# Kernel optimization log

Hardware: AMD Instinct MI355X
Metric: run time of the kernel (lower is better)

## Reference

```python
import jax, jax.numpy as jnp
import numpy as np

N, D, V, T = 2048, 64, 32000, 512
K_WTA = 256
X_DECAY, U_DECAY = 0.97, 0.97
SPIKE_RATE = 0.01
FORGET_ETA = 0.01
HOMEO_TAU = 1.0
GAMMA_MAX = 1.0


def ln_row(z, eps=1e-6):
    # torch .std is unbiased (ddof=1)
    m = z.mean(-1, keepdims=True)
    s = z.std(-1, ddof=1, keepdims=True)
    return (z - m) / (s + eps)


def setup_inputs() -> dict:
    key = jax.random.key(0)
    ks = jax.random.split(key, 6)
    return {
        "tokens": jax.random.randint(ks[0], (T,), 0, V),
        "spike_u": jax.random.uniform(ks[1], (T, N), dtype=jnp.float32),
        "E": jax.random.normal(ks[2], (D, N), dtype=jnp.float32) / np.sqrt(N).astype(np.float32),
        "Dx": jax.random.normal(ks[3], (N, D), dtype=jnp.float32) / np.sqrt(D).astype(np.float32),
        "Dy": jax.random.normal(ks[4], (N, D), dtype=jnp.float32) / np.sqrt(D).astype(np.float32),
        "token_emb": jax.random.normal(ks[5], (V, D), dtype=jnp.float32) / np.sqrt(D).astype(np.float32),
    }


def reference(tokens, spike_u, E, Dx, Dy, token_emb):
    def step(carry, inp):
        x, rho = carry
        tok, u = inp
        v_prev = token_emb[tok]                                   # (D,)
        x_t = X_DECAY * x + jax.nn.relu(Dx @ v_prev)              # (N,)
        x_t = x_t / (jnp.sum(jnp.abs(x_t)) + 1e-6)                # L1 normalize
        a_hat = ln_row(rho @ x_t)                                 # (D,) ln_before_Dy
        # branches=4 with elementwise softplus == softplus on full matvec
        y_core = jax.nn.softplus(Dy @ a_hat)                      # (N,)
        y_core = y_core + (u < SPIKE_RATE).astype(y_core.dtype)   # spike noise
        # k-WTA: keep top K_WTA entries
        _, idx = jax.lax.top_k(y_core, K_WTA)
        mask = jnp.zeros((N,), bool).at[idx].set(True)
        y_core = y_core * mask.astype(y_core.dtype)
        y_t = jax.nn.relu(y_core) * jax.nn.relu(x_t)
        # homeostasis (torch uses .item() -> constant scale)
        s = y_t.sum()
        scale = jnp.where(s > 1e-8, jnp.minimum(1.0, HOMEO_TAU / (s + 1e-8)), 1.0)
        y_t = y_t * jax.lax.stop_gradient(scale)
        v_star = ln_row(E @ y_t)                                  # (D,)
        # surprisal gain (torch uses .item() -> constant)
        p = jax.nn.softmax(v_star)
        H = -(p * jnp.log(p + 1e-12)).sum()
        gain = jnp.minimum(GAMMA_MAX, H / jnp.log(jnp.float32(D) + 1e-6) * GAMMA_MAX)
        gain = jax.lax.stop_gradient(gain)
        # dynamic top-k on x_t via rank masking (jit-safe data-dependent k)
        k_dyn = jnp.clip((N * (0.05 + 0.25 * gain)).astype(jnp.int32), 1, N)
        order = jnp.argsort(-x_t)
        ranks = jnp.zeros((N,), jnp.int32).at[order].set(jnp.arange(N, dtype=jnp.int32))
        x_t = x_t * (ranks < k_dyn).astype(x_t.dtype)
        # local forgetting on inactive columns, then Hebbian update
        inactive = (x_t <= 0).astype(rho.dtype)
        rho = rho * (1.0 - FORGET_ETA * inactive[None, :])
        rho = U_DECAY * (rho + gain * jnp.outer(v_prev, x_t))
        return (x_t, rho), v_star

    init = (jnp.zeros((N,), jnp.float32), jnp.zeros((D, N), jnp.float32))
    (_, _), v_stack = jax.lax.scan(step, init, (tokens, spike_u))
    return v_stack  # (T, D)
```

## Files before the change

### kernel.cpp

```cpp
#include <hip/hip_runtime.h>
#include <math.h>

#define NB   16
#define NTH  256
#define CH   128
#define NN   2048
#define DD   64
#define TT   512
#define KWTA 256
#define PA   65
#define PB   132

struct __align__(128) BarFlag { unsigned v; unsigned pad[31]; };
__device__ BarFlag g_flag[NB];
__device__ __align__(16) float  g_rf[NB][DD];
__device__ __align__(16) float  g_ef[NB][DD];
__device__ __align__(16) double g_L1[NB];
__device__ __align__(16) double g_s [NB];
__device__ __align__(16) float  g_xg[NN];
__device__ __align__(16) float  g_yg[NN];

__global__ void bdh_init() { if (threadIdx.x < NB) g_flag[threadIdx.x].v = 0u; }

__device__ __forceinline__ void grid_barrier(unsigned& epoch) {
  epoch += 1u;
  __syncthreads();
  if (threadIdx.x < 64) {
    if (threadIdx.x == 0) {
      __threadfence();
      __hip_atomic_store(&g_flag[blockIdx.x].v, epoch, __ATOMIC_RELAXED,
                         __HIP_MEMORY_SCOPE_AGENT);
    }
    const int i = (int)threadIdx.x;
    for (;;) {
      const bool ok = (i >= NB) ||
        (__hip_atomic_load(&g_flag[i].v, __ATOMIC_RELAXED,
                           __HIP_MEMORY_SCOPE_AGENT) >= epoch);
      if (__all(ok)) break;
      __builtin_amdgcn_s_sleep(1);
    }
    __builtin_amdgcn_fence(__ATOMIC_ACQUIRE, "agent");
  }
  __syncthreads();
}

__device__ __forceinline__ double wredd(double v) {
  #pragma unroll
  for (int off = 32; off > 0; off >>= 1) v += __shfl_xor(v, off, 64);
  return v;
}
__device__ __forceinline__ float wredf(float v) {
  #pragma unroll
  for (int off = 32; off > 0; off >>= 1) v += __shfl_xor(v, off, 64);
  return v;
}

__device__ void select_topk(const unsigned* __restrict__ keys, int K, int n0, int tid,
                            float* __restrict__ keep,
                            unsigned* __restrict__ hist,
                            unsigned* __restrict__ wsum,
                            int* __restrict__ misc)
{
  const int wave = tid >> 6, lane = tid & 63;
  const int sub = tid & 7;
  uint4* h4 = (uint4*)hist;
  unsigned prefix = 0u, pmask = 0u;
  int remK = K;
  for (int lev = 0; lev < 4; ++lev) {
    const int shf = 24 - 8*lev;
    const uint4 z = {0u,0u,0u,0u};
    h4[tid] = z; h4[tid + 256] = z;
    __syncthreads();
    #pragma unroll
    for (int j = 0; j < 8; ++j)
      if ((keys[j] & pmask) == prefix)
        atomicAdd(&hist[(((keys[j] >> shf) & 255u) << 3) + sub], 1u);
    __syncthreads();
    const uint4 a = h4[tid*2], bq = h4[tid*2 + 1];
    const unsigned c = a.x+a.y+a.z+a.w + bq.x+bq.y+bq.z+bq.w;
    unsigned s = c;
    #pragma unroll
    for (int off = 1; off < 64; off <<= 1) {
      unsigned o = __shfl_down(s, off, 64);
      if (lane + off < 64) s += o;
    }
    if (lane == 0) wsum[wave] = s;
    __syncthreads();
    unsigned hi = 0;
    for (int w = wave + 1; w < 4; ++w) hi += wsum[w];
    const unsigned A = s + hi;
    if (A >= (unsigned)remK && (A - c) < (unsigned)remK) {
      misc[0] = tid;
      misc[1] = remK - (int)(A - c);
    }
    __syncthreads();
    prefix |= ((unsigned)misc[0]) << shf;
    pmask  |= (255u << shf);
    remK = misc[1];
  }
  const unsigned thr = prefix;
  const unsigned R = (unsigned)remK;
  int lc[8]; int cnt = 0;
  #pragma unroll
  for (int j = 0; j < 8; ++j) { lc[j] = cnt; cnt += (keys[j] == thr) ? 1 : 0; }
  unsigned e = (unsigned)cnt;
  #pragma unroll
  for (int off = 1; off < 64; off <<= 1) {
    unsigned o = __shfl_up(e, off, 64);
    if (lane >= off) e += o;
  }
  if (lane == 63) wsum[4 + wave] = e;
  __syncthreads();
  unsigned base = 0;
  for (int w = 0; w < wave; ++w) base += wsum[4 + w];
  const unsigned excl = base + e - (unsigned)cnt;
  #pragma unroll
  for (int j = 0; j < 8; ++j) {
    const int g = tid*8 + j;
    const unsigned gg = (unsigned)(g - n0);
    if (gg < (unsigned)CH) {
      const bool kp = (keys[j] > thr) || ((keys[j] == thr) && (excl + (unsigned)lc[j] < R));
      keep[gg] = kp ? 1.0f : 0.0f;
    }
  }
  __syncthreads();
}

__global__ void __launch_bounds__(NTH)
bdh_main(const int* __restrict__ tokens, const float* __restrict__ spike_u,
         const float* __restrict__ Emat, const float* __restrict__ Dx,
         const float* __restrict__ Dy, const float* __restrict__ temb,
         float* __restrict__ out)
{
  __shared__ float sh_rho[DD][PB];
  __shared__ float sh_Dx[CH][PA];
  __shared__ float sh_Dy[CH][PA];
  __shared__ float sh_E [DD][PB];
  __shared__ int   sh_tok[TT];
  __shared__ float sh_v[2][DD];
  __shared__ float sh_xstate[CH];
  __shared__ float sh_xtun[CH];
  __shared__ float sh_xt[CH];
  __shared__ float sh_y[CH];
  __shared__ float sh_yt[CH];
  __shared__ float sh_ahat[DD];
  __shared__ float sh_keep[CH];
  __shared__ float sh_ffac[CH];
  __shared__ unsigned sh_hist[256*8];
  __shared__ unsigned sh_wsum[8];
  __shared__ int sh_misc[4];
  __shared__ float sh_fmisc[4];
  __shared__ double sh_dred[8];
  __shared__ double sh_rd[4][DD];

  const int tid  = threadIdx.x;
  const int b    = blockIdx.x;
  const int n0   = b * CH;
  const int i2   = tid >> 1;
  const int p2   = tid & 1;
  const int d4   = tid >> 2;
  const int p4   = tid & 3;
  const int lane = tid & 63;
  const int wv   = tid >> 6;
  unsigned epoch = 0u;

  for (int k = tid; k < TT; k += NTH) sh_tok[k] = tokens[k];
  for (int k = tid; k < DD*PB; k += NTH) (&sh_rho[0][0])[k] = 0.0f;
  if (tid < CH) sh_xstate[tid] = 0.0f;
  for (int r = wv; r < CH; r += 4) {
    sh_Dx[r][lane] = Dx[(size_t)(n0 + r)*DD + lane];
    sh_Dy[r][lane] = Dy[(size_t)(n0 + r)*DD + lane];
  }
  for (int r = wv; r < DD; r += 4) {
    sh_E[r][lane]      = Emat[(size_t)r*NN + n0 + lane];
    sh_E[r][lane + 64] = Emat[(size_t)r*NN + n0 + lane + 64];
  }
  __syncthreads();
  if (tid < DD) sh_v[0][tid] = temb[(size_t)sh_tok[0]*DD + tid];
  __syncthreads();

  for (int t = 0; t < TT; ++t) {
    const int par = t & 1;

    float spu = 0.0f;
    if (p2 == 0) spu = spike_u[(size_t)t*NN + n0 + i2];
    if (t + 1 < TT && tid < DD)
      sh_v[par ^ 1][tid] = temb[(size_t)sh_tok[t + 1]*DD + tid];

    float d1 = 0.0f;
    {
      const float* dxr = &sh_Dx[i2][p2*32];
      const float* vv  = &sh_v[par][p2*32];
      #pragma unroll
      for (int j = 0; j < 32; ++j) d1 += dxr[j] * vv[j];
    }
    d1 += __shfl_xor(d1, 1, 64);
    float xnew = 0.0f;
    if (p2 == 0) {
      xnew = 0.97f * sh_xstate[i2] + fmaxf(d1, 0.0f);
      sh_xtun[i2] = xnew;
    }
    {
      double v = (p2 == 0) ? (double)fabsf(xnew) : 0.0;
      v = wredd(v);
      if (lane == 0) sh_dred[wv] = v;
      __syncthreads();
      if (tid == 0) g_L1[b] = sh_dred[0] + sh_dred[1] + sh_dred[2] + sh_dred[3];
    }
    float qa = 0.0f;
    {
      const float* rr = &sh_rho[d4][0];
      #pragma unroll
      for (int j = 0; j < 32; ++j) { const int c = p4 + 4*j; qa += rr[c] * sh_xtun[c]; }
    }
    qa += __shfl_xor(qa, 1, 64);
    qa += __shfl_xor(qa, 2, 64);
    if (p4 == 0) g_rf[b][d4] = qa;
    grid_barrier(epoch);

    {
      double acc = 0.0;
      #pragma unroll
      for (int j = 0; j < 4; ++j) acc += (double)g_rf[(wv<<2) + j][lane];
      sh_rd[wv][lane] = acc;
    }
    if (tid < 64) {
      double v = (tid < NB) ? g_L1[tid] : 0.0;
      v = wredd(v);
      if (tid == 0) sh_dred[0] = v;
    }
    __syncthreads();
    const float Lden = (float)sh_dred[0] + 1e-6f;
    if (tid < 64) {
      const double qd = sh_rd[0][tid] + sh_rd[1][tid] + sh_rd[2][tid] + sh_rd[3][tid];
      const float rf = (float)qd / Lden;
      const float m  = wredf(rf) * (1.0f/64.0f);
      const float dv = rf - m;
      const float sd = sqrtf(wredf(dv*dv) * (1.0f/63.0f));
      sh_ahat[tid] = dv / (sd + 1e-6f);
    } else if (tid < 192) {
      const int l = tid - 64;
      const float xv = sh_xtun[l] / Lden;
      sh_xt[l] = xv;
      g_xg[n0 + l] = xv;
    }
    __syncthreads();
    float d2 = 0.0f;
    {
      const float* dyr = &sh_Dy[i2][p2*32];
      const float* aa  = &sh_ahat[p2*32];
      #pragma unroll
      for (int j = 0; j < 32; ++j) d2 += dyr[j] * aa[j];
    }
    d2 += __shfl_xor(d2, 1, 64);
    if (p2 == 0) {
      const float sp = fmaxf(d2, 0.0f) + log1pf(expf(-fabsf(d2)));
      const float y  = sp + ((spu < 0.01f) ? 1.0f : 0.0f);
      sh_y[i2] = y;
      g_yg[n0 + i2] = y;
    }
    grid_barrier(epoch);

    unsigned ykeys[8], xkeys[8];
    {
      const float4* py = ((const float4*)g_yg) + tid*2;
      const float4* px = ((const float4*)g_xg) + tid*2;
      float4 y0 = py[0], y1 = py[1];
      float4 x0 = px[0], x1 = px[1];
      ykeys[0]=__float_as_uint(y0.x); ykeys[1]=__float_as_uint(y0.y);
      ykeys[2]=__float_as_uint(y0.z); ykeys[3]=__float_as_uint(y0.w);
      ykeys[4]=__float_as_uint(y1.x); ykeys[5]=__float_as_uint(y1.y);
      ykeys[6]=__float_as_uint(y1.z); ykeys[7]=__float_as_uint(y1.w);
      xkeys[0]=__float_as_uint(x0.x); xkeys[1]=__float_as_uint(x0.y);
      xkeys[2]=__float_as_uint(x0.z); xkeys[3]=__float_as_uint(x0.w);
      xkeys[4]=__float_as_uint(x1.x); xkeys[5]=__float_as_uint(x1.y);
      xkeys[6]=__float_as_uint(x1.z); xkeys[7]=__float_as_uint(x1.w);
    }
    select_topk(ykeys, KWTA, n0, tid, sh_keep, sh_hist, sh_wsum, sh_misc);
    if (tid < CH) {
      const float ym = sh_keep[tid] * sh_y[tid];
      sh_yt[tid] = fmaxf(ym, 0.0f) * fmaxf(sh_xt[tid], 0.0f);
    }
    __syncthreads();
    float ea = 0.0f;
    {
      const float* er = &sh_E[d4][0];
      #pragma unroll
      for (int j = 0; j < 32; ++j) { const int c = p4 + 4*j; ea += er[c] * sh_yt[c]; }
    }
    ea += __shfl_xor(ea, 1, 64);
    ea += __shfl_xor(ea, 2, 64);
    if (p4 == 0) g_ef[b][d4] = ea;
    {
      double v = (tid < CH) ? (double)sh_yt[tid] : 0.0;
      v = wredd(v);
      if (lane == 0) sh_dred[4 + wv] = v;
      __syncthreads();
      if (tid == 0) g_s[b] = sh_dred[4] + sh_dred[5] + sh_dred[6] + sh_dred[7];
    }
    grid_barrier(epoch);

    {
      double acc = 0.0;
      #pragma unroll
      for (int j = 0; j < 4; ++j) acc += (double)g_ef[(wv<<2) + j][lane];
      sh_rd[wv][lane] = acc;
    }
    if (tid < 64) {
      double v = (tid < NB) ? g_s[tid] : 0.0;
      v = wredd(v);
      if (tid == 0) sh_dred[0] = v;
    }
    __syncthreads();
    const float sf = (float)sh_dred[0];
    const float scale = (sf > 1e-8f) ? fminf(1.0f, 1.0f/(sf + 1e-8f)) : 1.0f;
    if (tid < 64) {
      const double ed = sh_rd[0][tid] + sh_rd[1][tid] + sh_rd[2][tid] + sh_rd[3][tid];
      const float z = scale * (float)ed;
      const float m  = wredf(z) * (1.0f/64.0f);
      const float dv = z - m;
      const float sd = sqrtf(wredf(dv*dv) * (1.0f/63.0f));
      const float vs = dv / (sd + 1e-6f);
      if (b == 0) out[t*DD + tid] = vs;
      float mx = vs;
      #pragma unroll
      for (int off = 32; off > 0; off >>= 1) mx = fmaxf(mx, __shfl_xor(mx, off, 64));
      const float ex = expf(vs - mx);
      const float se = wredf(ex);
      const float pp = ex / se;
      const float ht = wredf(-pp * logf(pp + 1e-12f));
      if (tid == 0) sh_fmisc[0] = fminf(1.0f, ht / logf(64.0f));
    }
    __syncthreads();
    const float gain = sh_fmisc[0];
    int kd = (int)(2048.0f * (0.05f + 0.25f * gain));
    kd = kd < 1 ? 1 : (kd > NN ? NN : kd);
    select_topk(xkeys, kd, n0, tid, sh_keep, sh_hist, sh_wsum, sh_misc);
    if (tid < CH) {
      const float xm = sh_keep[tid] * sh_xt[tid];
      sh_xstate[tid] = xm;
      sh_ffac[tid] = (xm <= 0.0f) ? (1.0f - 0.01f) : 1.0f;
    }
    __syncthreads();
    {
      const float vd = sh_v[par][d4];
      float* rr = &sh_rho[d4][0];
      #pragma unroll
      for (int j = 0; j < 32; ++j) {
        const int c = p4 + 4*j;
        rr[c] = 0.97f * (rr[c]*sh_ffac[c] + gain * (vd * sh_xstate[c]));
      }
    }
    __syncthreads();
  }
}

extern "C" void kernel_launch(void* const* d_in, const int* in_sizes, int n_in,
                              void* d_out, int out_size, void* d_ws, size_t ws_size,
                              hipStream_t stream) {
  const int*   tokens = (const int*)d_in[0];
  const float* spike  = (const float*)d_in[1];
  const float* Emat   = (const float*)d_in[2];
  const float* Dx     = (const float*)d_in[3];
  const float* Dy     = (const float*)d_in[4];
  const float* temb   = (const float*)d_in[5];
  float* out = (float*)d_out;
  (void)in_sizes; (void)n_in; (void)out_size; (void)d_ws; (void)ws_size;
  bdh_init<<<dim3(1), dim3(64), 0, stream>>>();
  bdh_main<<<dim3(NB), dim3(NTH), 0, stream>>>(tokens, spike, Emat, Dx, Dy, temb, out);
}
```

Before: 9.784 ms.

## Compute E@y redundantly per block to drop a grid barrier per step

Each block now computes the full k-WTA selection and the sparse E@y_t product itself: it gathers at most 256 active columns from a transposed copy of E that the init kernel writes to global memory, so the second grid barrier and its cross-block reductions per timestep go away. The radix top-k selection is also restructured to double-buffer its histogram, cutting it to 4 bins per bucket and using a ballot to find the threshold, which removes several block syncs per level. The cost is redundant gather work in every block and reads of E from global or L2 memory instead of LDS.

```diff
diff --git a/kernel.cpp b/kernel.cpp
--- a/kernel.cpp
+++ b/kernel.cpp
@@ -14,13 +14,19 @@
 struct __align__(128) BarFlag { unsigned v; unsigned pad[31]; };
 __device__ BarFlag g_flag[NB];
 __device__ __align__(16) float  g_rf[NB][DD];
-__device__ __align__(16) float  g_ef[NB][DD];
 __device__ __align__(16) double g_L1[NB];
-__device__ __align__(16) double g_s [NB];
 __device__ __align__(16) float  g_xg[NN];
 __device__ __align__(16) float  g_yg[NN];
-
-__global__ void bdh_init() { if (threadIdx.x < NB) g_flag[threadIdx.x].v = 0u; }
+__device__ __align__(16) float  g_ET[NN*DD];
+
+__global__ void bdh_init(const float* __restrict__ E) {
+  const int gid = blockIdx.x * NTH + threadIdx.x;
+  if (gid < NB) g_flag[gid].v = 0u;
+  for (int idx = gid; idx < NN * DD; idx += 64 * NTH) {
+    const int n = idx >> 6, d = idx & 63;
+    g_ET[idx] = E[(size_t)d * NN + n];
+  }
+}
 
 __device__ __forceinline__ void grid_barrier(unsigned& epoch) {
   epoch += 1u;
@@ -55,75 +61,78 @@
   return v;
 }
 
-__device__ void select_topk(const unsigned* __restrict__ keys, int K, int n0, int tid,
-                            float* __restrict__ keep,
-                            unsigned* __restrict__ hist,
-                            unsigned* __restrict__ wsum,
-                            int* __restrict__ misc)
+__device__ __forceinline__ unsigned select_mask(const unsigned* __restrict__ keys,
+                                                int K, int tid,
+                                                unsigned* __restrict__ hist,
+                                                unsigned* __restrict__ cw)
 {
-  const int wave = tid >> 6, lane = tid & 63;
-  const int sub = tid & 7;
-  uint4* h4 = (uint4*)hist;
+  const int wv = tid >> 6, lane = tid & 63;
+  uint4* H4 = (uint4*)hist;
+  const uint4 z4 = {0u, 0u, 0u, 0u};
+  H4[tid] = z4;
   unsigned prefix = 0u, pmask = 0u;
-  int remK = K;
+  int remK = K, buf = 0;
+  __syncthreads();
+  #pragma unroll
   for (int lev = 0; lev < 4; ++lev) {
-    const int shf = 24 - 8*lev;
-    const uint4 z = {0u,0u,0u,0u};
-    h4[tid] = z; h4[tid + 256] = z;
-    __syncthreads();
+    const int shf = 24 - 8 * lev;
     #pragma unroll
     for (int j = 0; j < 8; ++j)
       if ((keys[j] & pmask) == prefix)
-        atomicAdd(&hist[(((keys[j] >> shf) & 255u) << 3) + sub], 1u);
-    __syncthreads();
-    const uint4 a = h4[tid*2], bq = h4[tid*2 + 1];
-    const unsigned c = a.x+a.y+a.z+a.w + bq.x+bq.y+bq.z+bq.w;
-    unsigned s = c;
+        atomicAdd(&hist[buf * 1024 + (((keys[j] >> shf) & 255u) << 2) + wv], 1u);
+    __syncthreads();
+    unsigned c[4], s[4];
+    #pragma unroll
+    for (int k = 0; k < 4; ++k) {
+      const uint4 h = H4[buf * 256 + 4 * lane + k];
+      c[k] = h.x + h.y + h.z + h.w;
+    }
+    s[3] = c[3]; s[2] = c[2] + s[3]; s[1] = c[1] + s[2]; s[0] = c[0] + s[1];
+    unsigned SS = s[0];
     #pragma unroll
     for (int off = 1; off < 64; off <<= 1) {
-      unsigned o = __shfl_down(s, off, 64);
-      if (lane + off < 64) s += o;
-    }
-    if (lane == 0) wsum[wave] = s;
-    __syncthreads();
-    unsigned hi = 0;
-    for (int w = wave + 1; w < 4; ++w) hi += wsum[w];
-    const unsigned A = s + hi;
-    if (A >= (unsigned)remK && (A - c) < (unsigned)remK) {
-      misc[0] = tid;
-      misc[1] = remK - (int)(A - c);
-    }
-    __syncthreads();
-    prefix |= ((unsigned)misc[0]) << shf;
-    pmask  |= (255u << shf);
-    remK = misc[1];
+      const unsigned o = __shfl_down(SS, off, 64);
+      if (lane + off < 64) SS += o;
+    }
+    const unsigned T = SS - s[0];
+    unsigned pk = 0u;
+    #pragma unroll
+    for (int k = 0; k < 4; ++k) {
+      const unsigned A = s[k] + T;
+      if (A >= (unsigned)remK && (A - c[k]) < (unsigned)remK)
+        pk = (((unsigned)(4 * lane + k)) << 16) | (unsigned)(remK - (int)(A - c[k]));
+    }
+    const unsigned long long bal = __ballot(pk != 0u);
+    const int src = __ffsll(bal) - 1;
+    pk = __shfl(pk, src, 64);
+    prefix |= (pk >> 16) << shf;
+    remK = (int)(pk & 0xffffu);
+    pmask |= 255u << shf;
+    H4[(buf ^ 1) * 256 + tid] = z4;
+    buf ^= 1;
+    __syncthreads();
   }
   const unsigned thr = prefix;
   const unsigned R = (unsigned)remK;
-  int lc[8]; int cnt = 0;
-  #pragma unroll
-  for (int j = 0; j < 8; ++j) { lc[j] = cnt; cnt += (keys[j] == thr) ? 1 : 0; }
-  unsigned e = (unsigned)cnt;
+  unsigned lc[8], cnt = 0u;
+  #pragma unroll
+  for (int j = 0; j < 8; ++j) { lc[j] = cnt; cnt += (keys[j] == thr) ? 1u : 0u; }
+  unsigned e = cnt;
   #pragma unroll
   for (int off = 1; off < 64; off <<= 1) {
-    unsigned o = __shfl_up(e, off, 64);
+    const unsigned o = __shfl_up(e, off, 64);
     if (lane >= off) e += o;
   }
-  if (lane == 63) wsum[4 + wave] = e;
-  __syncthreads();
-  unsigned base = 0;
-  for (int w = 0; w < wave; ++w) base += wsum[4 + w];
-  const unsigned excl = base + e - (unsigned)cnt;
-  #pragma unroll
-  for (int j = 0; j < 8; ++j) {
-    const int g = tid*8 + j;
-    const unsigned gg = (unsigned)(g - n0);
-    if (gg < (unsigned)CH) {
-      const bool kp = (keys[j] > thr) || ((keys[j] == thr) && (excl + (unsigned)lc[j] < R));
-      keep[gg] = kp ? 1.0f : 0.0f;
-    }
-  }
-  __syncthreads();
+  if (lane == 63) cw[wv] = e;
+  __syncthreads();
+  unsigned base = 0u;
+  for (int w = 0; w < wv; ++w) base += cw[w];
+  const unsigned excl = base + e - cnt;
+  unsigned mask = 0u;
+  #pragma unroll
+  for (int j = 0; j < 8; ++j)
+    if (keys[j] > thr || (keys[j] == thr && excl + lc[j] < R)) mask |= 1u << j;
+  return mask;
 }
 
 __global__ void __launch_bounds__(NTH)
@@ -135,23 +144,20 @@
   __shared__ float sh_rho[DD][PB];
   __shared__ float sh_Dx[CH][PA];
   __shared__ float sh_Dy[CH][PA];
-  __shared__ float sh_E [DD][PB];
   __shared__ int   sh_tok[TT];
   __shared__ float sh_v[2][DD];
   __shared__ float sh_xstate[CH];
   __shared__ float sh_xtun[CH];
-  __shared__ float sh_xt[CH];
-  __shared__ float sh_y[CH];
-  __shared__ float sh_yt[CH];
   __shared__ float sh_ahat[DD];
-  __shared__ float sh_keep[CH];
   __shared__ float sh_ffac[CH];
-  __shared__ unsigned sh_hist[256*8];
-  __shared__ unsigned sh_wsum[8];
-  __shared__ int sh_misc[4];
+  __shared__ unsigned sh_hist[2][256][4];
+  __shared__ unsigned sh_cw[8];
   __shared__ float sh_fmisc[4];
   __shared__ double sh_dred[8];
   __shared__ double sh_rd[4][DD];
+  __shared__ float sh_gred[4][DD];
+  __shared__ int   sh_aidx[KWTA];
+  __shared__ float sh_aw[KWTA];
 
   const int tid  = threadIdx.x;
   const int b    = blockIdx.x;
@@ -171,10 +177,6 @@
     sh_Dx[r][lane] = Dx[(size_t)(n0 + r)*DD + lane];
     sh_Dy[r][lane] = Dy[(size_t)(n0 + r)*DD + lane];
   }
-  for (int r = wv; r < DD; r += 4) {
-    sh_E[r][lane]      = Emat[(size_t)r*NN + n0 + lane];
-    sh_E[r][lane + 64] = Emat[(size_t)r*NN + n0 + lane + 64];
-  }
   __syncthreads();
   if (tid < DD) sh_v[0][tid] = temb[(size_t)sh_tok[0]*DD + tid];
   __syncthreads();
@@ -240,9 +242,7 @@
       sh_ahat[tid] = dv / (sd + 1e-6f);
     } else if (tid < 192) {
       const int l = tid - 64;
-      const float xv = sh_xtun[l] / Lden;
-      sh_xt[l] = xv;
-      g_xg[n0 + l] = xv;
+      g_xg[n0 + l] = sh_xtun[l] / Lden;
     }
     __syncthreads();
     float d2 = 0.0f;
@@ -255,9 +255,7 @@
     d2 += __shfl_xor(d2, 1, 64);
     if (p2 == 0) {
       const float sp = fmaxf(d2, 0.0f) + log1pf(expf(-fabsf(d2)));
-      const float y  = sp + ((spu < 0.01f) ? 1.0f : 0.0f);
-      sh_y[i2] = y;
-      g_yg[n0 + i2] = y;
+      g_yg[n0 + i2] = sp + ((spu < 0.01f) ? 1.0f : 0.0f);
     }
     grid_barrier(epoch);
 
@@ -265,8 +263,8 @@
     {
       const float4* py = ((const float4*)g_yg) + tid*2;
       const float4* px = ((const float4*)g_xg) + tid*2;
-      float4 y0 = py[0], y1 = py[1];
-      float4 x0 = px[0], x1 = px[1];
+      const float4 y0 = py[0], y1 = py[1];
+      const float4 x0 = px[0], x1 = px[1];
       ykeys[0]=__float_as_uint(y0.x); ykeys[1]=__float_as_uint(y0.y);
       ykeys[2]=__float_as_uint(y0.z); ykeys[3]=__float_as_uint(y0.w);
       ykeys[4]=__float_as_uint(y1.x); ykeys[5]=__float_as_uint(y1.y);
@@ -276,49 +274,59 @@
       xkeys[4]=__float_as_uint(x1.x); xkeys[5]=__float_as_uint(x1.y);
       xkeys[6]=__float_as_uint(x1.z); xkeys[7]=__float_as_uint(x1.w);
     }
-    select_topk(ykeys, KWTA, n0, tid, sh_keep, sh_hist, sh_wsum, sh_misc);
-    if (tid < CH) {
-      const float ym = sh_keep[tid] * sh_y[tid];
-      sh_yt[tid] = fmaxf(ym, 0.0f) * fmaxf(sh_xt[tid], 0.0f);
-    }
-    __syncthreads();
-    float ea = 0.0f;
-    {
-      const float* er = &sh_E[d4][0];
-      #pragma unroll
-      for (int j = 0; j < 32; ++j) { const int c = p4 + 4*j; ea += er[c] * sh_yt[c]; }
-    }
-    ea += __shfl_xor(ea, 1, 64);
-    ea += __shfl_xor(ea, 2, 64);
-    if (p4 == 0) g_ef[b][d4] = ea;
-    {
-      double v = (tid < CH) ? (double)sh_yt[tid] : 0.0;
-      v = wredd(v);
-      if (lane == 0) sh_dred[4 + wv] = v;
-      __syncthreads();
-      if (tid == 0) g_s[b] = sh_dred[4] + sh_dred[5] + sh_dred[6] + sh_dred[7];
-    }
-    grid_barrier(epoch);
-
-    {
-      double acc = 0.0;
-      #pragma unroll
-      for (int j = 0; j < 4; ++j) acc += (double)g_ef[(wv<<2) + j][lane];
-      sh_rd[wv][lane] = acc;
-    }
+    const unsigned km = select_mask(ykeys, KWTA, tid, &sh_hist[0][0][0], sh_cw);
+    float p[8]; unsigned nzm = 0u;
+    #pragma unroll
+    for (int j = 0; j < 8; ++j) {
+      const float yv = __uint_as_float(ykeys[j]);
+      const float xv = __uint_as_float(xkeys[j]);
+      p[j] = yv * xv;
+      if (((km >> j) & 1u) && xv > 0.0f) nzm |= 1u << j;
+    }
+    const unsigned cnt = (unsigned)__popc(nzm);
+    {
+      double sp = 0.0;
+      #pragma unroll
+      for (int j = 0; j < 8; ++j) if ((nzm >> j) & 1u) sp += (double)p[j];
+      sp = wredd(sp);
+      if (lane == 0) sh_dred[wv] = sp;
+    }
+    unsigned e = cnt;
+    #pragma unroll
+    for (int off = 1; off < 64; off <<= 1) {
+      const unsigned o = __shfl_up(e, off, 64);
+      if (lane >= off) e += o;
+    }
+    if (lane == 63) sh_cw[4 + wv] = e;
+    __syncthreads();
+    const float sf = (float)(sh_dred[0] + sh_dred[1] + sh_dred[2] + sh_dred[3]);
+    const float scale = (sf > 1e-8f) ? fminf(1.0f, 1.0f/(sf + 1e-8f)) : 1.0f;
+    const int m = (int)(sh_cw[4] + sh_cw[5] + sh_cw[6] + sh_cw[7]);
+    {
+      unsigned base = 0u;
+      for (int w = 0; w < wv; ++w) base += sh_cw[4 + w];
+      int pos = (int)(base + e - cnt);
+      #pragma unroll
+      for (int j = 0; j < 8; ++j)
+        if ((nzm >> j) & 1u) { sh_aidx[pos] = 8*tid + j; sh_aw[pos] = scale * p[j]; ++pos; }
+    }
+    __syncthreads();
+    {
+      float a0 = 0.0f, a1 = 0.0f;
+      int i = wv;
+      for (; i + 4 < m; i += 8) {
+        a0 = fmaf(sh_aw[i],     g_ET[(size_t)sh_aidx[i]*DD + lane],     a0);
+        a1 = fmaf(sh_aw[i + 4], g_ET[(size_t)sh_aidx[i + 4]*DD + lane], a1);
+      }
+      for (; i < m; i += 4)
+        a0 = fmaf(sh_aw[i], g_ET[(size_t)sh_aidx[i]*DD + lane], a0);
+      sh_gred[wv][lane] = a0 + a1;
+    }
+    __syncthreads();
     if (tid < 64) {
-      double v = (tid < NB) ? g_s[tid] : 0.0;
-      v = wredd(v);
-      if (tid == 0) sh_dred[0] = v;
-    }
-    __syncthreads();
-    const float sf = (float)sh_dred[0];
-    const float scale = (sf > 1e-8f) ? fminf(1.0f, 1.0f/(sf + 1e-8f)) : 1.0f;
-    if (tid < 64) {
-      const double ed = sh_rd[0][tid] + sh_rd[1][tid] + sh_rd[2][tid] + sh_rd[3][tid];
-      const float z = scale * (float)ed;
-      const float m  = wredf(z) * (1.0f/64.0f);
-      const float dv = z - m;
+      const float z = sh_gred[0][tid] + sh_gred[1][tid] + sh_gred[2][tid] + sh_gred[3][tid];
+      const float mn = wredf(z) * (1.0f/64.0f);
+      const float dv = z - mn;
       const float sd = sqrtf(wredf(dv*dv) * (1.0f/63.0f));
       const float vs = dv / (sd + 1e-6f);
       if (b == 0) out[t*DD + tid] = vs;
@@ -335,11 +343,17 @@
     const float gain = sh_fmisc[0];
     int kd = (int)(2048.0f * (0.05f + 0.25f * gain));
     kd = kd < 1 ? 1 : (kd > NN ? NN : kd);
-    select_topk(xkeys, kd, n0, tid, sh_keep, sh_hist, sh_wsum, sh_misc);
-    if (tid < CH) {
-      const float xm = sh_keep[tid] * sh_xt[tid];
-      sh_xstate[tid] = xm;
-      sh_ffac[tid] = (xm <= 0.0f) ? (1.0f - 0.01f) : 1.0f;
+    const unsigned xm = select_mask(xkeys, kd, tid, &sh_hist[0][0][0], sh_cw);
+    #pragma unroll
+    for (int j = 0; j < 8; ++j) {
+      const int g = 8*tid + j;
+      const unsigned l = (unsigned)(g - n0);
+      if (l < (unsigned)CH) {
+        const float xv = __uint_as_float(xkeys[j]);
+        const float v = ((xm >> j) & 1u) ? xv : 0.0f;
+        sh_xstate[l] = v;
+        sh_ffac[l] = (v <= 0.0f) ? (1.0f - 0.01f) : 1.0f;
+      }
     }
     __syncthreads();
     {
@@ -366,6 +380,6 @@
   const float* temb   = (const float*)d_in[5];
   float* out = (float*)d_out;
   (void)in_sizes; (void)n_in; (void)out_size; (void)d_ws; (void)ws_size;
-  bdh_init<<<dim3(1), dim3(64), 0, stream>>>();
+  bdh_init<<<dim3(64), dim3(NTH), 0, stream>>>(Emat);
   bdh_main<<<dim3(NB), dim3(NTH), 0, stream>>>(tokens, spike, Emat, Dx, Dy, temb, out);
 }
```

Measured after the change: 11.37 ms. +16.2%, slower.
